# Performance work log

Hardware: AMD Instinct MI355X
Metric: run time of the kernel (lower is better)

## Reference

```python
import jax, jax.numpy as jnp
import numpy as np

N, C, K, H = 131072, 512, 128, 8  # points, channels, patch_size, heads


def setup_inputs() -> dict:
    key = jax.random.key(0)
    ks = jax.random.split(key, 6)
    feat = jax.random.normal(ks[0], (N, C), dtype=jnp.float32)
    Wqkv = jax.random.normal(ks[1], (C, 3 * C), dtype=jnp.float32) * 0.02
    bqkv = jax.random.normal(ks[2], (3 * C,), dtype=jnp.float32) * 0.02
    Wproj = jax.random.normal(ks[3], (C, C), dtype=jnp.float32) * 0.02
    bproj = jax.random.normal(ks[4], (C,), dtype=jnp.float32) * 0.02
    order = jax.random.permutation(ks[5], N).astype(jnp.int64)  # serialized order (all clusters full)
    inverse = jnp.argsort(order).astype(jnp.int64)              # serialized inverse
    return {"feat": feat, "Wqkv": Wqkv, "bqkv": bqkv, "Wproj": Wproj,
            "bproj": bproj, "order": order, "inverse": inverse}


def reference(feat, Wqkv, bqkv, Wproj, bproj, order, inverse):
    hd = C // H
    scale = hd ** -0.5
    qkv = feat @ Wqkv + bqkv                 # [N, 3C]
    qkv = qkv[order]                         # gather by serialized order
    qkv = qkv.reshape(-1, K, 3, H, hd)       # [W, K, 3, H, hd]
    qkv = jnp.moveaxis(qkv, 2, 0)            # [3, W, K, H, hd]
    q = jnp.swapaxes(qkv[0], 1, 2)           # [W, H, K, hd]
    k = jnp.swapaxes(qkv[1], 1, 2)
    v = jnp.swapaxes(qkv[2], 1, 2)
    # upcast_attention / upcast_softmax -> compute scores & softmax in fp32
    attn = jnp.einsum('whkd,whjd->whkj', (q * scale).astype(jnp.float32),
                      k.astype(jnp.float32))             # [W, H, K, K]
    attn = jax.nn.softmax(attn, axis=-1).astype(feat.dtype)
    out = jnp.einsum('whkj,whjd->whkd', attn, v)          # [W, H, K, hd]
    out = jnp.swapaxes(out, 1, 2).reshape(-1, C)          # [N, C]
    out = out[inverse]                                    # scatter back via inverse
    out = out @ Wproj + bproj
    return out
```

## Files before the change

### kernel.cpp

```cpp
#include <hip/hip_runtime.h>
#include <hip/hip_bf16.h>
#include <cstdint>
#include <cstddef>

typedef __bf16 bf16;
typedef __bf16 bf16x8 __attribute__((ext_vector_type(8)));
typedef float f32x4 __attribute__((ext_vector_type(4)));

#define N_PTS 131072
#define CDIM  512
#define C3    1536
#define HD    64
#define NH    8
#define KWIN  128

static __device__ __forceinline__ bf16 cvt(float x) { return (bf16)x; }

static __device__ __forceinline__ void gld16(const bf16* g, bf16* l) {
    __builtin_amdgcn_global_load_lds(
        (const __attribute__((address_space(1))) void*)g,
        (__attribute__((address_space(3))) void*)l, 16, 0, 0);
}

__global__ __launch_bounds__(256) void k_prep(
    const float* __restrict__ Wqkv, const float* __restrict__ Wproj,
    bf16* __restrict__ Wqkv_t, bf16* __restrict__ Wproj_t)
{
    int idx = blockIdx.x * 256 + threadIdx.x;
    if (idx < CDIM * C3) {
        int k = idx / C3, c = idx % C3;
        Wqkv_t[(size_t)c * CDIM + k] = cvt(Wqkv[idx]);
    } else {
        int j = idx - CDIM * C3;
        if (j < CDIM * CDIM) {
            int k = j / CDIM, c = j % CDIM;
            Wproj_t[(size_t)c * CDIM + k] = cvt(Wproj[j]);
        }
    }
}

__global__ __launch_bounds__(256) void k_gather(
    const float* __restrict__ feat, const int* __restrict__ order,
    bf16* __restrict__ feat_g)
{
    int row = blockIdx.x * 2 + (threadIdx.x >> 7);
    int c   = (threadIdx.x & 127) << 2;
    int src = order[row];
    float4 v = *reinterpret_cast<const float4*>(feat + (size_t)src * CDIM + c);
    union { bf16 e[4]; uint2 u; } pk;
    pk.e[0] = cvt(v.x); pk.e[1] = cvt(v.y); pk.e[2] = cvt(v.z); pk.e[3] = cvt(v.w);
    *reinterpret_cast<uint2*>(feat_g + (size_t)row * CDIM + c) = pk.u;
}

template <bool F32OUT, int NT>
__global__ __launch_bounds__(512, 4) void k_gemm(
    const bf16* __restrict__ Ag, const bf16* __restrict__ Bt,
    const float* __restrict__ bias, void* __restrict__ outp)
{
    __shared__ __align__(16) bf16 As[2][128 * 32];
    __shared__ __align__(16) bf16 Bs[2][256 * 32];

    const int t    = threadIdx.x;
    const int lane = t & 63;
    const int wv   = t >> 6;
    const int wr   = wv >> 2;
    const int wc   = wv & 3;
    const int g    = lane >> 4, r16 = lane & 15;

    const int nwg = gridDim.x;
    const int bid = blockIdx.x;
    const int swz = (bid & 7) * (nwg >> 3) + (bid >> 3);
    const int m0  = (swz / NT) * 128;
    const int n0  = (swz % NT) * 256;

    const int L0 = wv * 64 + lane;
    const int rA = L0 >> 2,          sA = ((L0 & 3) - (rA >> 1)) & 3;
    const int rB1 = rA + 128,        sB1v = ((L0 & 3) - (rB1 >> 1)) & 3;
    const bf16* srcA  = Ag + (size_t)(m0 + rA) * CDIM + sA * 8;
    const bf16* srcB0 = Bt + (size_t)(n0 + rA) * CDIM + sA * 8;
    const bf16* srcB1 = Bt + (size_t)(n0 + rB1) * CDIM + sB1v * 8;

    int aoff[4], boff[4];
#pragma unroll
    for (int m = 0; m < 4; ++m) {
        int row = wr * 64 + m * 16 + r16;
        aoff[m] = row * 64 + (((g + (row >> 1)) & 3) << 4);
    }
#pragma unroll
    for (int n = 0; n < 4; ++n) {
        int row = wc * 64 + n * 16 + r16;
        boff[n] = row * 64 + (((g + (row >> 1)) & 3) << 4);
    }

    f32x4 acc[4][4];
    const f32x4 z = {0.f, 0.f, 0.f, 0.f};
#pragma unroll
    for (int m = 0; m < 4; ++m)
#pragma unroll
        for (int n = 0; n < 4; ++n) acc[m][n] = z;

    auto stage = [&](int kt) {
        const int b  = kt & 1;
        const int ko = kt * 32;
        gld16(srcA  + ko, &As[b][(size_t)wv * 64 * 8]);
        gld16(srcB0 + ko, &Bs[b][(size_t)wv * 64 * 8]);
        gld16(srcB1 + ko, &Bs[b][(size_t)(512 + wv * 64) * 8]);
    };

    auto compute = [&](int kt) {
        const int b = kt & 1;
        bf16x8 af[4], bv[4];
#pragma unroll
        for (int m = 0; m < 4; ++m)
            af[m] = *reinterpret_cast<const bf16x8*>(
                reinterpret_cast<const char*>(&As[b][0]) + aoff[m]);
#pragma unroll
        for (int n = 0; n < 4; ++n)
            bv[n] = *reinterpret_cast<const bf16x8*>(
                reinterpret_cast<const char*>(&Bs[b][0]) + boff[n]);
        __builtin_amdgcn_s_setprio(1);
#pragma unroll
        for (int m = 0; m < 4; ++m)
#pragma unroll
            for (int n = 0; n < 4; ++n)
                acc[m][n] = __builtin_amdgcn_mfma_f32_16x16x32_bf16(
                    af[m], bv[n], acc[m][n], 0, 0, 0);
        __builtin_amdgcn_s_setprio(0);
    };

    const int NKT = CDIM / 32;

    stage(0); stage(1);
    asm volatile("s_waitcnt vmcnt(3)" ::: "memory");
    __builtin_amdgcn_s_barrier();

#pragma unroll
    for (int kt = 0; kt < NKT - 2; ++kt) {
        compute(kt);
        asm volatile("s_waitcnt lgkmcnt(0)" ::: "memory");
        __builtin_amdgcn_s_barrier();
        stage(kt + 2);
        asm volatile("s_waitcnt vmcnt(3)" ::: "memory");
        __builtin_amdgcn_s_barrier();
    }
    compute(NKT - 2);
    asm volatile("s_waitcnt vmcnt(0) lgkmcnt(0)" ::: "memory");
    __builtin_amdgcn_s_barrier();
    compute(NKT - 1);

    const int ldo = NT * 256;
#pragma unroll
    for (int n = 0; n < 4; ++n) {
        int col = n0 + wc * 64 + n * 16 + r16;
        float b = bias[col];
#pragma unroll
        for (int m = 0; m < 4; ++m)
#pragma unroll
            for (int j = 0; j < 4; ++j) {
                int row = m0 + wr * 64 + m * 16 + g * 4 + j;
                if (F32OUT)
                    reinterpret_cast<float*>(outp)[(size_t)row * ldo + col] =
                        acc[m][n][j] + b;
                else
                    reinterpret_cast<bf16*>(outp)[(size_t)row * ldo + col] =
                        cvt(acc[m][n][j] + b);
            }
    }
}

__global__ __launch_bounds__(256) void k_attn(
    const bf16* __restrict__ qkv_s, const int* __restrict__ order,
    bf16* __restrict__ attn_g)
{
    __shared__ __align__(16) char smem[36864 + 64 * 136 * 2];
    __shared__ int ord_s[KWIN];
    bf16 (*Q)[72]   = reinterpret_cast<bf16 (*)[72]>(smem);
    bf16 (*Kt)[72]  = reinterpret_cast<bf16 (*)[72]>(smem + 128 * 72 * 2);
    bf16 (*P)[136]  = reinterpret_cast<bf16 (*)[136]>(smem);
    bf16 (*Vt)[136] = reinterpret_cast<bf16 (*)[136]>(smem + 36864);

    const int t    = threadIdx.x;
    const int lane = t & 63;
    const int wv   = t >> 6;
    const int g    = lane >> 4, r16 = lane & 15;
    const int h    = blockIdx.x;
    const int w    = blockIdx.y;

    const bf16* base = qkv_s + (size_t)w * KWIN * C3 + h * HD;

    if (t < KWIN) ord_s[t] = order[w * KWIN + t];

#pragma unroll
    for (int it = 0; it < 4; ++it) {
        int s   = it * 256 + t;
        int tok = s >> 3;
        int c8  = (s & 7) << 3;
        size_t roff = (size_t)tok * C3 + c8;
        *reinterpret_cast<uint4*>(&Q[tok][c8])  =
            *reinterpret_cast<const uint4*>(base + roff);
        *reinterpret_cast<uint4*>(&Kt[tok][c8]) =
            *reinterpret_cast<const uint4*>(base + roff + CDIM);
        uint4 vvec = *reinterpret_cast<const uint4*>(base + roff + 2 * CDIM);
        const bf16* ve = reinterpret_cast<const bf16*>(&vvec);
#pragma unroll
        for (int i = 0; i < 8; ++i) Vt[c8 + i][tok] = ve[i];
    }
    __syncthreads();

    f32x4 sc[2][8];
    const f32x4 z = {0.f, 0.f, 0.f, 0.f};
#pragma unroll
    for (int m = 0; m < 2; ++m)
#pragma unroll
        for (int n = 0; n < 8; ++n) sc[m][n] = z;

#pragma unroll
    for (int ks = 0; ks < 2; ++ks) {
        bf16x8 aq[2];
#pragma unroll
        for (int m = 0; m < 2; ++m)
            aq[m] = *reinterpret_cast<const bf16x8*>(
                &Q[wv * 32 + m * 16 + r16][ks * 32 + g * 8]);
#pragma unroll
        for (int n = 0; n < 8; ++n) {
            bf16x8 bk = *reinterpret_cast<const bf16x8*>(
                &Kt[n * 16 + r16][ks * 32 + g * 8]);
#pragma unroll
            for (int m = 0; m < 2; ++m)
                sc[m][n] = __builtin_amdgcn_mfma_f32_16x16x32_bf16(
                    aq[m], bk, sc[m][n], 0, 0, 0);
        }
    }

    const float scale = 0.125f;
    float inv_sum[2][4];
#pragma unroll
    for (int m = 0; m < 2; ++m) {
#pragma unroll
        for (int j = 0; j < 4; ++j) {
            float mx = -3.0e38f;
#pragma unroll
            for (int n = 0; n < 8; ++n) mx = fmaxf(mx, sc[m][n][j]);
            mx = fmaxf(mx, __shfl_xor(mx, 1));
            mx = fmaxf(mx, __shfl_xor(mx, 2));
            mx = fmaxf(mx, __shfl_xor(mx, 4));
            mx = fmaxf(mx, __shfl_xor(mx, 8));
            mx *= scale;
            float ssum = 0.f;
#pragma unroll
            for (int n = 0; n < 8; ++n) {
                float p = __expf(sc[m][n][j] * scale - mx);
                sc[m][n][j] = p;
                ssum += p;
            }
            ssum += __shfl_xor(ssum, 1);
            ssum += __shfl_xor(ssum, 2);
            ssum += __shfl_xor(ssum, 4);
            ssum += __shfl_xor(ssum, 8);
            inv_sum[m][j] = 1.f / ssum;
        }
    }

    __syncthreads();

#pragma unroll
    for (int m = 0; m < 2; ++m)
#pragma unroll
        for (int n = 0; n < 8; ++n)
#pragma unroll
            for (int j = 0; j < 4; ++j)
                P[wv * 32 + m * 16 + g * 4 + j][n * 16 + r16] =
                    cvt(sc[m][n][j] * inv_sum[m][j]);

    f32x4 o[2][4];
#pragma unroll
    for (int m = 0; m < 2; ++m)
#pragma unroll
        for (int n = 0; n < 4; ++n) o[m][n] = z;

#pragma unroll
    for (int kt = 0; kt < 4; ++kt) {
        bf16x8 ap[2];
#pragma unroll
        for (int m = 0; m < 2; ++m)
            ap[m] = *reinterpret_cast<const bf16x8*>(
                &P[wv * 32 + m * 16 + r16][kt * 32 + g * 8]);
#pragma unroll
        for (int n = 0; n < 4; ++n) {
            bf16x8 bv = *reinterpret_cast<const bf16x8*>(
                &Vt[n * 16 + r16][kt * 32 + g * 8]);
#pragma unroll
            for (int m = 0; m < 2; ++m)
                o[m][n] = __builtin_amdgcn_mfma_f32_16x16x32_bf16(
                    ap[m], bv, o[m][n], 0, 0, 0);
        }
    }

#pragma unroll
    for (int m = 0; m < 2; ++m)
#pragma unroll
        for (int n = 0; n < 4; ++n)
#pragma unroll
            for (int j = 0; j < 4; ++j) {
                int tok  = wv * 32 + m * 16 + g * 4 + j;
                int d    = n * 16 + r16;
                int drow = ord_s[tok];
                attn_g[(size_t)drow * CDIM + h * HD + d] = cvt(o[m][n][j]);
            }
}

extern "C" void kernel_launch(void* const* d_in, const int* in_sizes, int n_in,
                              void* d_out, int out_size, void* d_ws, size_t ws_size,
                              hipStream_t stream)
{
    const float* feat    = (const float*)d_in[0];
    const float* Wqkv    = (const float*)d_in[1];
    const float* bqkv    = (const float*)d_in[2];
    const float* Wproj   = (const float*)d_in[3];
    const float* bproj   = (const float*)d_in[4];
    const int*   order   = (const int*)d_in[5];
    float* out = (float*)d_out;

    const size_t qkv_bytes  = (size_t)N_PTS * C3 * sizeof(bf16);
    const size_t gat_bytes  = (size_t)N_PTS * CDIM * sizeof(bf16);
    const size_t wq_bytes   = (size_t)C3 * CDIM * sizeof(bf16);
    const size_t wp_bytes   = (size_t)CDIM * CDIM * sizeof(bf16);
    if (ws_size < qkv_bytes + gat_bytes + wq_bytes + wp_bytes) return;

    bf16* qkv_s     = (bf16*)d_ws;
    bf16* shared134 = (bf16*)((char*)d_ws + qkv_bytes);
    bf16* Wqkv_t    = (bf16*)((char*)d_ws + qkv_bytes + gat_bytes);
    bf16* Wproj_t   = (bf16*)((char*)d_ws + qkv_bytes + gat_bytes + wq_bytes);

    k_prep<<<dim3((CDIM * C3 + CDIM * CDIM + 255) / 256), 256, 0, stream>>>(
        Wqkv, Wproj, Wqkv_t, Wproj_t);
    k_gather<<<dim3(N_PTS / 2), 256, 0, stream>>>(feat, order, shared134);
    k_gemm<false, C3 / 256><<<dim3((N_PTS / 128) * (C3 / 256)), 512, 0, stream>>>(
        shared134, Wqkv_t, bqkv, qkv_s);
    k_attn<<<dim3(NH, N_PTS / KWIN), 256, 0, stream>>>(qkv_s, order, shared134);
    k_gemm<true, CDIM / 256><<<dim3((N_PTS / 128) * (CDIM / 256)), 512, 0, stream>>>(
        shared134, Wproj_t, bproj, out);
}
```

Before: 640.1 us.

## Fuse row gather and fp32-to-bf16 conversion into QKV GEMM A-tile loading

```diff
diff --git a/kernel.cpp b/kernel.cpp
--- a/kernel.cpp
+++ b/kernel.cpp
@@ -39,26 +39,15 @@
     }
 }
 
-__global__ __launch_bounds__(256) void k_gather(
-    const float* __restrict__ feat, const int* __restrict__ order,
-    bf16* __restrict__ feat_g)
-{
-    int row = blockIdx.x * 2 + (threadIdx.x >> 7);
-    int c   = (threadIdx.x & 127) << 2;
-    int src = order[row];
-    float4 v = *reinterpret_cast<const float4*>(feat + (size_t)src * CDIM + c);
-    union { bf16 e[4]; uint2 u; } pk;
-    pk.e[0] = cvt(v.x); pk.e[1] = cvt(v.y); pk.e[2] = cvt(v.z); pk.e[3] = cvt(v.w);
-    *reinterpret_cast<uint2*>(feat_g + (size_t)row * CDIM + c) = pk.u;
-}
-
-template <bool F32OUT, int NT>
+template <bool GATHER, bool F32OUT, int NT>
 __global__ __launch_bounds__(512, 4) void k_gemm(
-    const bf16* __restrict__ Ag, const bf16* __restrict__ Bt,
-    const float* __restrict__ bias, void* __restrict__ outp)
+    const void* __restrict__ Ag_, const bf16* __restrict__ Bt,
+    const float* __restrict__ bias, const int* __restrict__ order,
+    void* __restrict__ outp)
 {
     __shared__ __align__(16) bf16 As[2][128 * 32];
     __shared__ __align__(16) bf16 Bs[2][256 * 32];
+    __shared__ int ord_s[128];
 
     const int t    = threadIdx.x;
     const int lane = t & 63;
@@ -73,12 +62,25 @@
     const int m0  = (swz / NT) * 128;
     const int n0  = (swz % NT) * 256;
 
-    const int L0 = wv * 64 + lane;
-    const int rA = L0 >> 2,          sA = ((L0 & 3) - (rA >> 1)) & 3;
-    const int rB1 = rA + 128,        sB1v = ((L0 & 3) - (rB1 >> 1)) & 3;
-    const bf16* srcA  = Ag + (size_t)(m0 + rA) * CDIM + sA * 8;
-    const bf16* srcB0 = Bt + (size_t)(n0 + rA) * CDIM + sA * 8;
-    const bf16* srcB1 = Bt + (size_t)(n0 + rB1) * CDIM + sB1v * 8;
+    const float* Af = (const float*)Ag_;
+    const bf16*  Ab = (const bf16*)Ag_;
+    const int NKT = CDIM / 32;
+
+    if (GATHER) {
+        if (t < 128) ord_s[t] = order[m0 + t];
+        __syncthreads();
+    }
+
+    const int rowA = t >> 2;
+    const int ksA  = ((t & 3) - (rowA >> 1)) & 3;
+    const float* gsrcA = GATHER
+        ? Af + (size_t)ord_s[rowA] * CDIM + ksA * 8 : nullptr;
+    const bf16* srcA_l = Ab + (size_t)(m0 + rowA) * CDIM + ksA * 8;
+
+    const int rB0 = t >> 2,        sB0 = ((t & 3) - (rB0 >> 1)) & 3;
+    const int rB1 = rB0 + 128,     sB1 = ((t & 3) - (rB1 >> 1)) & 3;
+    const bf16* srcB0 = Bt + (size_t)(n0 + rB0) * CDIM + sB0 * 8;
+    const bf16* srcB1 = Bt + (size_t)(n0 + rB1) * CDIM + sB1 * 8;
 
     int aoff[4], boff[4];
 #pragma unroll
@@ -99,54 +101,91 @@
 #pragma unroll
         for (int n = 0; n < 4; ++n) acc[m][n] = z;
 
-    auto stage = [&](int kt) {
-        const int b  = kt & 1;
-        const int ko = kt * 32;
-        gld16(srcA  + ko, &As[b][(size_t)wv * 64 * 8]);
-        gld16(srcB0 + ko, &Bs[b][(size_t)wv * 64 * 8]);
-        gld16(srcB1 + ko, &Bs[b][(size_t)(512 + wv * 64) * 8]);
+    auto stageB = [&](int s) {
+        const int b = s & 1;
+        gld16(srcB0 + s * 32, &Bs[b][(size_t)wv * 64 * 8]);
+        gld16(srcB1 + s * 32, &Bs[b][(size_t)(512 + wv * 64) * 8]);
     };
-
-    auto compute = [&](int kt) {
-        const int b = kt & 1;
-        bf16x8 af[4], bv[4];
+    auto stageA_l = [&](int s) {
+        const int b = s & 1;
+        gld16(srcA_l + s * 32, &As[b][(size_t)wv * 64 * 8]);
+    };
+    auto packA = [&](int s, float4 fa, float4 fb) {
+        union { bf16 e[8]; uint4 u; } pk;
+        pk.e[0] = cvt(fa.x); pk.e[1] = cvt(fa.y);
+        pk.e[2] = cvt(fa.z); pk.e[3] = cvt(fa.w);
+        pk.e[4] = cvt(fb.x); pk.e[5] = cvt(fb.y);
+        pk.e[6] = cvt(fb.z); pk.e[7] = cvt(fb.w);
+        *reinterpret_cast<uint4*>(
+            reinterpret_cast<char*>(&As[s & 1][0]) + t * 16) = pk.u;
+    };
+    auto compute = [&](int s) {
+        const int b = s & 1;
+        const char* ab = reinterpret_cast<const char*>(&As[b][0]);
+        const char* bb = reinterpret_cast<const char*>(&Bs[b][0]);
+        bf16x8 af[4], bvv[4];
 #pragma unroll
         for (int m = 0; m < 4; ++m)
-            af[m] = *reinterpret_cast<const bf16x8*>(
-                reinterpret_cast<const char*>(&As[b][0]) + aoff[m]);
+            af[m] = *reinterpret_cast<const bf16x8*>(ab + aoff[m]);
 #pragma unroll
         for (int n = 0; n < 4; ++n)
-            bv[n] = *reinterpret_cast<const bf16x8*>(
-                reinterpret_cast<const char*>(&Bs[b][0]) + boff[n]);
+            bvv[n] = *reinterpret_cast<const bf16x8*>(bb + boff[n]);
         __builtin_amdgcn_s_setprio(1);
 #pragma unroll
         for (int m = 0; m < 4; ++m)
 #pragma unroll
             for (int n = 0; n < 4; ++n)
                 acc[m][n] = __builtin_amdgcn_mfma_f32_16x16x32_bf16(
-                    af[m], bv[n], acc[m][n], 0, 0, 0);
+                    af[m], bvv[n], acc[m][n], 0, 0, 0);
         __builtin_amdgcn_s_setprio(0);
     };
 
-    const int NKT = CDIM / 32;
-
-    stage(0); stage(1);
-    asm volatile("s_waitcnt vmcnt(3)" ::: "memory");
-    __builtin_amdgcn_s_barrier();
-
-#pragma unroll
-    for (int kt = 0; kt < NKT - 2; ++kt) {
-        compute(kt);
+    if (GATHER) {
+        float4 fa0 = *reinterpret_cast<const float4*>(gsrcA);
+        float4 fb0 = *reinterpret_cast<const float4*>(gsrcA + 4);
+        float4 fa1 = *reinterpret_cast<const float4*>(gsrcA + 32);
+        float4 fb1 = *reinterpret_cast<const float4*>(gsrcA + 36);
+        stageB(0); stageB(1);
+        packA(0, fa0, fb0);
+        packA(1, fa1, fb1);
+        asm volatile("s_waitcnt vmcnt(2) lgkmcnt(0)" ::: "memory");
+        __builtin_amdgcn_s_barrier();
+    } else {
+        stageA_l(0); stageB(0);
+        stageA_l(1); stageB(1);
+        asm volatile("s_waitcnt vmcnt(3)" ::: "memory");
+        __builtin_amdgcn_s_barrier();
+    }
+
+#pragma unroll
+    for (int s = 0; s < NKT; ++s) {
+        float4 fa, fb;
+        if (GATHER && s + 2 < NKT) {
+            fa = *reinterpret_cast<const float4*>(gsrcA + (s + 2) * 32);
+            fb = *reinterpret_cast<const float4*>(gsrcA + (s + 2) * 32 + 4);
+        }
+        compute(s);
+        if (s == NKT - 1) break;
         asm volatile("s_waitcnt lgkmcnt(0)" ::: "memory");
         __builtin_amdgcn_s_barrier();
-        stage(kt + 2);
-        asm volatile("s_waitcnt vmcnt(3)" ::: "memory");
+        if (GATHER) {
+            if (s + 2 < NKT) {
+                packA(s + 2, fa, fb);
+                stageB(s + 2);
+                asm volatile("s_waitcnt lgkmcnt(0)" ::: "memory");
+            } else {
+                asm volatile("s_waitcnt vmcnt(0)" ::: "memory");
+            }
+        } else {
+            if (s + 2 < NKT) {
+                stageA_l(s + 2); stageB(s + 2);
+                asm volatile("s_waitcnt vmcnt(3)" ::: "memory");
+            } else {
+                asm volatile("s_waitcnt vmcnt(0)" ::: "memory");
+            }
+        }
         __builtin_amdgcn_s_barrier();
     }
-    compute(NKT - 2);
-    asm volatile("s_waitcnt vmcnt(0) lgkmcnt(0)" ::: "memory");
-    __builtin_amdgcn_s_barrier();
-    compute(NKT - 1);
 
     const int ldo = NT * 256;
 #pragma unroll
@@ -287,12 +326,12 @@
                 &P[wv * 32 + m * 16 + r16][kt * 32 + g * 8]);
 #pragma unroll
         for (int n = 0; n < 4; ++n) {
-            bf16x8 bv = *reinterpret_cast<const bf16x8*>(
+            bf16x8 bvv = *reinterpret_cast<const bf16x8*>(
                 &Vt[n * 16 + r16][kt * 32 + g * 8]);
 #pragma unroll
             for (int m = 0; m < 2; ++m)
                 o[m][n] = __builtin_amdgcn_mfma_f32_16x16x32_bf16(
-                    ap[m], bv, o[m][n], 0, 0, 0);
+                    ap[m], bvv, o[m][n], 0, 0, 0);
         }
     }
 
@@ -327,17 +366,18 @@
     const size_t wp_bytes   = (size_t)CDIM * CDIM * sizeof(bf16);
     if (ws_size < qkv_bytes + gat_bytes + wq_bytes + wp_bytes) return;
 
-    bf16* qkv_s     = (bf16*)d_ws;
-    bf16* shared134 = (bf16*)((char*)d_ws + qkv_bytes);
-    bf16* Wqkv_t    = (bf16*)((char*)d_ws + qkv_bytes + gat_bytes);
-    bf16* Wproj_t   = (bf16*)((char*)d_ws + qkv_bytes + gat_bytes + wq_bytes);
+    bf16* qkv_s   = (bf16*)d_ws;
+    bf16* attn_g  = (bf16*)((char*)d_ws + qkv_bytes);
+    bf16* Wqkv_t  = (bf16*)((char*)d_ws + qkv_bytes + gat_bytes);
+    bf16* Wproj_t = (bf16*)((char*)d_ws + qkv_bytes + gat_bytes + wq_bytes);
 
     k_prep<<<dim3((CDIM * C3 + CDIM * CDIM + 255) / 256), 256, 0, stream>>>(
         Wqkv, Wproj, Wqkv_t, Wproj_t);
-    k_gather<<<dim3(N_PTS / 2), 256, 0, stream>>>(feat, order, shared134);
-    k_gemm<false, C3 / 256><<<dim3((N_PTS / 128) * (C3 / 256)), 512, 0, stream>>>(
-        shared134, Wqkv_t, bqkv, qkv_s);
-    k_attn<<<dim3(NH, N_PTS / KWIN), 256, 0, stream>>>(qkv_s, order, shared134);
-    k_gemm<true, CDIM / 256><<<dim3((N_PTS / 128) * (CDIM / 256)), 512, 0, stream>>>(
-        shared134, Wproj_t, bproj, out);
-}
+    k_gemm<true, false, C3 / 256>
+        <<<dim3((N_PTS / 128) * (C3 / 256)), 512, 0, stream>>>(
+        feat, Wqkv_t, bqkv, order, qkv_s);
+    k_attn<<<dim3(NH, N_PTS / KWIN), 256, 0, stream>>>(qkv_s, order, attn_g);
+    k_gemm<false, true, CDIM / 256>
+        <<<dim3((N_PTS / 128) * (CDIM / 256)), 512, 0, stream>>>(
+        attn_g, Wproj_t, bproj, order, out);
+}
```

Result: faster. 598.0 us (-6.6%).

## Restructure GEMM to 128x128 tiles with triple-buffered LDS and register prefetch

Applied to the files above, without the earlier changes.

```diff
diff --git a/kernel.cpp b/kernel.cpp
--- a/kernel.cpp
+++ b/kernel.cpp
@@ -53,32 +53,34 @@
 }
 
 template <bool F32OUT, int NT>
-__global__ __launch_bounds__(512, 4) void k_gemm(
+__global__ __launch_bounds__(256, 3) void k_gemm(
     const bf16* __restrict__ Ag, const bf16* __restrict__ Bt,
     const float* __restrict__ bias, void* __restrict__ outp)
 {
-    __shared__ __align__(16) bf16 As[2][128 * 32];
-    __shared__ __align__(16) bf16 Bs[2][256 * 32];
+    __shared__ __align__(16) bf16 As[3][128 * 32];
+    __shared__ __align__(16) bf16 Bs[3][128 * 32];
 
     const int t    = threadIdx.x;
     const int lane = t & 63;
     const int wv   = t >> 6;
-    const int wr   = wv >> 2;
-    const int wc   = wv & 3;
+    const int wr   = wv >> 1;
+    const int wc   = wv & 1;
     const int g    = lane >> 4, r16 = lane & 15;
 
     const int nwg = gridDim.x;
     const int bid = blockIdx.x;
     const int swz = (bid & 7) * (nwg >> 3) + (bid >> 3);
     const int m0  = (swz / NT) * 128;
-    const int n0  = (swz % NT) * 256;
-
-    const int L0 = wv * 64 + lane;
-    const int rA = L0 >> 2,          sA = ((L0 & 3) - (rA >> 1)) & 3;
-    const int rB1 = rA + 128,        sB1v = ((L0 & 3) - (rB1 >> 1)) & 3;
-    const bf16* srcA  = Ag + (size_t)(m0 + rA) * CDIM + sA * 8;
-    const bf16* srcB0 = Bt + (size_t)(n0 + rA) * CDIM + sA * 8;
-    const bf16* srcB1 = Bt + (size_t)(n0 + rB1) * CDIM + sB1v * 8;
+    const int n0  = (swz % NT) * 128;
+
+    const int NKT = CDIM / 32;
+
+    const int r0 = t >> 2,       s0 = ((t & 3) - (r0 >> 1)) & 3;
+    const int r1 = r0 + 64,      s1 = ((t & 3) - (r1 >> 1)) & 3;
+    const bf16* srcA0 = Ag + (size_t)(m0 + r0) * CDIM + s0 * 8;
+    const bf16* srcA1 = Ag + (size_t)(m0 + r1) * CDIM + s1 * 8;
+    const bf16* srcB0 = Bt + (size_t)(n0 + r0) * CDIM + s0 * 8;
+    const bf16* srcB1 = Bt + (size_t)(n0 + r1) * CDIM + s1 * 8;
 
     int aoff[4], boff[4];
 #pragma unroll
@@ -99,56 +101,58 @@
 #pragma unroll
         for (int n = 0; n < 4; ++n) acc[m][n] = z;
 
-    auto stage = [&](int kt) {
-        const int b  = kt & 1;
-        const int ko = kt * 32;
-        gld16(srcA  + ko, &As[b][(size_t)wv * 64 * 8]);
-        gld16(srcB0 + ko, &Bs[b][(size_t)wv * 64 * 8]);
-        gld16(srcB1 + ko, &Bs[b][(size_t)(512 + wv * 64) * 8]);
+    auto stage = [&](int s) {
+        const int b  = s % 3;
+        const int ko = s * 32;
+        gld16(srcA0 + ko, &As[b][(size_t)(wv * 64) * 8]);
+        gld16(srcA1 + ko, &As[b][(size_t)(wv * 64 + 256) * 8]);
+        gld16(srcB0 + ko, &Bs[b][(size_t)(wv * 64) * 8]);
+        gld16(srcB1 + ko, &Bs[b][(size_t)(wv * 64 + 256) * 8]);
     };
 
-    auto compute = [&](int kt) {
-        const int b = kt & 1;
-        bf16x8 af[4], bv[4];
+    bf16x8 afr[2][4], bfr[2][4];
+
+    auto ldfrags = [&](int set, int b) {
+        const char* ab = reinterpret_cast<const char*>(&As[b][0]);
+        const char* bb = reinterpret_cast<const char*>(&Bs[b][0]);
 #pragma unroll
         for (int m = 0; m < 4; ++m)
-            af[m] = *reinterpret_cast<const bf16x8*>(
-                reinterpret_cast<const char*>(&As[b][0]) + aoff[m]);
+            afr[set][m] = *reinterpret_cast<const bf16x8*>(ab + aoff[m]);
 #pragma unroll
         for (int n = 0; n < 4; ++n)
-            bv[n] = *reinterpret_cast<const bf16x8*>(
-                reinterpret_cast<const char*>(&Bs[b][0]) + boff[n]);
+            bfr[set][n] = *reinterpret_cast<const bf16x8*>(bb + boff[n]);
+    };
+
+    stage(0); stage(1);
+    asm volatile("s_waitcnt vmcnt(4)" ::: "memory");
+    __builtin_amdgcn_s_barrier();
+    ldfrags(0, 0);
+    asm volatile("s_waitcnt lgkmcnt(0)" ::: "memory");
+
+#pragma unroll
+    for (int s = 0; s < NKT; ++s) {
+        if (s + 2 < NKT) stage(s + 2);
+        if (s < NKT - 1) {
+            if (s + 2 < NKT)
+                asm volatile("s_waitcnt vmcnt(4)" ::: "memory");
+            else
+                asm volatile("s_waitcnt vmcnt(0)" ::: "memory");
+            __builtin_amdgcn_s_barrier();
+            ldfrags((s + 1) & 1, (s + 1) % 3);
+        }
         __builtin_amdgcn_s_setprio(1);
 #pragma unroll
         for (int m = 0; m < 4; ++m)
 #pragma unroll
             for (int n = 0; n < 4; ++n)
                 acc[m][n] = __builtin_amdgcn_mfma_f32_16x16x32_bf16(
-                    af[m], bv[n], acc[m][n], 0, 0, 0);
+                    afr[s & 1][m], bfr[s & 1][n], acc[m][n], 0, 0, 0);
         __builtin_amdgcn_s_setprio(0);
-    };
-
-    const int NKT = CDIM / 32;
-
-    stage(0); stage(1);
-    asm volatile("s_waitcnt vmcnt(3)" ::: "memory");
-    __builtin_amdgcn_s_barrier();
-
-#pragma unroll
-    for (int kt = 0; kt < NKT - 2; ++kt) {
-        compute(kt);
-        asm volatile("s_waitcnt lgkmcnt(0)" ::: "memory");
-        __builtin_amdgcn_s_barrier();
-        stage(kt + 2);
-        asm volatile("s_waitcnt vmcnt(3)" ::: "memory");
-        __builtin_amdgcn_s_barrier();
-    }
-    compute(NKT - 2);
-    asm volatile("s_waitcnt vmcnt(0) lgkmcnt(0)" ::: "memory");
-    __builtin_amdgcn_s_barrier();
-    compute(NKT - 1);
-
-    const int ldo = NT * 256;
+        if (s < NKT - 1)
+            asm volatile("s_waitcnt lgkmcnt(0)" ::: "memory");
+    }
+
+    const int ldo = NT * 128;
 #pragma unroll
     for (int n = 0; n < 4; ++n) {
         int col = n0 + wc * 64 + n * 16 + r16;
@@ -287,12 +291,12 @@
                 &P[wv * 32 + m * 16 + r16][kt * 32 + g * 8]);
 #pragma unroll
         for (int n = 0; n < 4; ++n) {
-            bf16x8 bv = *reinterpret_cast<const bf16x8*>(
+            bf16x8 bvv = *reinterpret_cast<const bf16x8*>(
                 &Vt[n * 16 + r16][kt * 32 + g * 8]);
 #pragma unroll
             for (int m = 0; m < 2; ++m)
                 o[m][n] = __builtin_amdgcn_mfma_f32_16x16x32_bf16(
-                    ap[m], bv, o[m][n], 0, 0, 0);
+                    ap[m], bvv, o[m][n], 0, 0, 0);
         }
     }
 
@@ -321,10 +325,10 @@
     const int*   order   = (const int*)d_in[5];
     float* out = (float*)d_out;
 
-    const size_t qkv_bytes  = (size_t)N_PTS * C3 * sizeof(bf16);
-    const size_t gat_bytes  = (size_t)N_PTS * CDIM * sizeof(bf16);
-    const size_t wq_bytes   = (size_t)C3 * CDIM * sizeof(bf16);
-    const size_t wp_bytes   = (size_t)CDIM * CDIM * sizeof(bf16);
+    const size_t qkv_bytes = (size_t)N_PTS * C3 * sizeof(bf16);
+    const size_t gat_bytes = (size_t)N_PTS * CDIM * sizeof(bf16);
+    const size_t wq_bytes  = (size_t)C3 * CDIM * sizeof(bf16);
+    const size_t wp_bytes  = (size_t)CDIM * CDIM * sizeof(bf16);
     if (ws_size < qkv_bytes + gat_bytes + wq_bytes + wp_bytes) return;
 
     bf16* qkv_s     = (bf16*)d_ws;
@@ -335,9 +339,9 @@
     k_prep<<<dim3((CDIM * C3 + CDIM * CDIM + 255) / 256), 256, 0, stream>>>(
         Wqkv, Wproj, Wqkv_t, Wproj_t);
     k_gather<<<dim3(N_PTS / 2), 256, 0, stream>>>(feat, order, shared134);
-    k_gemm<false, C3 / 256><<<dim3((N_PTS / 128) * (C3 / 256)), 512, 0, stream>>>(
+    k_gemm<false, C3 / 128><<<dim3((N_PTS / 128) * (C3 / 128)), 256, 0, stream>>>(
         shared134, Wqkv_t, bqkv, qkv_s);
     k_attn<<<dim3(NH, N_PTS / KWIN), 256, 0, stream>>>(qkv_s, order, shared134);
-    k_gemm<true, CDIM / 256><<<dim3((N_PTS / 128) * (CDIM / 256)), 512, 0, stream>>>(
+    k_gemm<true, CDIM / 128><<<dim3((N_PTS / 128) * (CDIM / 128)), 256, 0, stream>>>(
         shared134, Wproj_t, bproj, out);
 }
```

After: 671.3 us. 1.05x slower.

## Pre-swizzle QKV GEMM operands into MFMA fragment layout and load directly to registers

Applied to the files above, without the earlier changes.

```diff
diff --git a/kernel.cpp b/kernel.cpp
--- a/kernel.cpp
+++ b/kernel.cpp
@@ -13,6 +13,7 @@
 #define HD    64
 #define NH    8
 #define KWIN  128
+#define NKS   16
 
 static __device__ __forceinline__ bf16 cvt(float x) { return (bf16)x; }
 
@@ -22,34 +23,120 @@
         (__attribute__((address_space(3))) void*)l, 16, 0, 0);
 }
 
+
 __global__ __launch_bounds__(256) void k_prep(
     const float* __restrict__ Wqkv, const float* __restrict__ Wproj,
-    bf16* __restrict__ Wqkv_t, bf16* __restrict__ Wproj_t)
-{
-    int idx = blockIdx.x * 256 + threadIdx.x;
-    if (idx < CDIM * C3) {
-        int k = idx / C3, c = idx % C3;
-        Wqkv_t[(size_t)c * CDIM + k] = cvt(Wqkv[idx]);
+    bf16* __restrict__ Wq_frag, bf16* __restrict__ Wp_t)
+{
+    const int b = blockIdx.x, t = threadIdx.x;
+    if (b < 384) {
+        int slot  = b * 256 + t;
+        int chunk = slot >> 6;
+        int l     = slot & 63;
+        int cf = chunk >> 4, ks = chunk & 15;
+        int col = cf * 16 + (l & 15);
+        int kb  = ks * 32 + (l >> 4) * 8;
+        union { bf16 e[8]; uint4 u; } pk;
+#pragma unroll
+        for (int ei = 0; ei < 8; ++ei)
+            pk.e[ei] = cvt(Wqkv[(size_t)(kb + ei) * C3 + col]);
+        *reinterpret_cast<uint4*>(Wq_frag + (size_t)chunk * 512 + l * 8) = pk.u;
     } else {
-        int j = idx - CDIM * C3;
-        if (j < CDIM * CDIM) {
-            int k = j / CDIM, c = j % CDIM;
-            Wproj_t[(size_t)c * CDIM + k] = cvt(Wproj[j]);
-        }
+        int j = (b - 384) * 256 + t;
+        int k = j >> 9, c = j & 511;
+        Wp_t[(size_t)c * CDIM + k] = cvt(Wproj[(size_t)k * CDIM + c]);
     }
 }
 
 __global__ __launch_bounds__(256) void k_gather(
     const float* __restrict__ feat, const int* __restrict__ order,
-    bf16* __restrict__ feat_g)
-{
-    int row = blockIdx.x * 2 + (threadIdx.x >> 7);
-    int c   = (threadIdx.x & 127) << 2;
-    int src = order[row];
-    float4 v = *reinterpret_cast<const float4*>(feat + (size_t)src * CDIM + c);
-    union { bf16 e[4]; uint2 u; } pk;
-    pk.e[0] = cvt(v.x); pk.e[1] = cvt(v.y); pk.e[2] = cvt(v.z); pk.e[3] = cvt(v.w);
-    *reinterpret_cast<uint2*>(feat_g + (size_t)row * CDIM + c) = pk.u;
+    bf16* __restrict__ Afrag)
+{
+    const int rf = blockIdx.x;
+    const int t = threadIdx.x, wv = t >> 6, l = t & 63;
+    const int srow = order[rf * 16 + (l & 15)];
+    const float* src = feat + (size_t)srow * CDIM + (l >> 4) * 8;
+#pragma unroll
+    for (int q = 0; q < 4; ++q) {
+        int ks = wv * 4 + q;
+        float4 v0 = *reinterpret_cast<const float4*>(src + ks * 32);
+        float4 v1 = *reinterpret_cast<const float4*>(src + ks * 32 + 4);
+        union { bf16 e[8]; uint4 u; } pk;
+        pk.e[0] = cvt(v0.x); pk.e[1] = cvt(v0.y);
+        pk.e[2] = cvt(v0.z); pk.e[3] = cvt(v0.w);
+        pk.e[4] = cvt(v1.x); pk.e[5] = cvt(v1.y);
+        pk.e[6] = cvt(v1.z); pk.e[7] = cvt(v1.w);
+        *reinterpret_cast<uint4*>(
+            Afrag + ((size_t)rf * 16 + ks) * 512 + l * 8) = pk.u;
+    }
+}
+
+template <int NT>
+__global__ __launch_bounds__(512, 2) void k_mm_frag(
+    const bf16* __restrict__ Afrag, const bf16* __restrict__ Bfrag,
+    const float* __restrict__ bias, bf16* __restrict__ outp)
+{
+    const int t    = threadIdx.x;
+    const int lane = t & 63;
+    const int wv   = t >> 6;
+    const int wr   = wv >> 2;
+    const int wc   = wv & 3;
+    const int g    = lane >> 4, r16 = lane & 15;
+
+    const int nwg = gridDim.x;
+    const int bid = blockIdx.x;
+    const int swz = (bid & 7) * (nwg >> 3) + (bid >> 3);
+    const int m0  = (swz / NT) * 256;
+    const int n0  = (swz % NT) * 256;
+
+    const bf16* pA = Afrag + (size_t)(m0 / 16 + wr * 8) * 8192 + lane * 8;
+    const bf16* pB = Bfrag + (size_t)(n0 / 16 + wc * 4) * 8192 + lane * 8;
+
+    f32x4 acc[8][4];
+    const f32x4 z = {0.f, 0.f, 0.f, 0.f};
+#pragma unroll
+    for (int i = 0; i < 8; ++i)
+#pragma unroll
+        for (int n = 0; n < 4; ++n) acc[i][n] = z;
+
+    bf16x8 aR[2][8], bR[2][4];
+
+    auto LD = [&](int set, int ks) {
+#pragma unroll
+        for (int i = 0; i < 8; ++i)
+            aR[set][i] = *reinterpret_cast<const bf16x8*>(pA + i * 8192 + ks * 512);
+#pragma unroll
+        for (int n = 0; n < 4; ++n)
+            bR[set][n] = *reinterpret_cast<const bf16x8*>(pB + n * 8192 + ks * 512);
+    };
+
+    LD(0, 0);
+#pragma unroll
+    for (int ks = 0; ks < NKS; ++ks) {
+        if (ks + 1 < NKS) LD((ks + 1) & 1, ks + 1);
+        __builtin_amdgcn_s_setprio(1);
+#pragma unroll
+        for (int i = 0; i < 8; ++i)
+#pragma unroll
+            for (int n = 0; n < 4; ++n)
+                acc[i][n] = __builtin_amdgcn_mfma_f32_16x16x32_bf16(
+                    aR[ks & 1][i], bR[ks & 1][n], acc[i][n], 0, 0, 0);
+        __builtin_amdgcn_s_setprio(0);
+    }
+
+    const int ldo = NT * 256;
+#pragma unroll
+    for (int n = 0; n < 4; ++n) {
+        int col = n0 + wc * 64 + n * 16 + r16;
+        float b = bias[col];
+#pragma unroll
+        for (int i = 0; i < 8; ++i)
+#pragma unroll
+            for (int j = 0; j < 4; ++j) {
+                int row = m0 + wr * 128 + i * 16 + g * 4 + j;
+                outp[(size_t)row * ldo + col] = cvt(acc[i][n][j] + b);
+            }
+    }
 }
 
 template <bool F32OUT, int NT>
@@ -109,14 +196,14 @@
 
     auto compute = [&](int kt) {
         const int b = kt & 1;
-        bf16x8 af[4], bv[4];
+        bf16x8 af[4], bvv[4];
 #pragma unroll
         for (int m = 0; m < 4; ++m)
             af[m] = *reinterpret_cast<const bf16x8*>(
                 reinterpret_cast<const char*>(&As[b][0]) + aoff[m]);
 #pragma unroll
         for (int n = 0; n < 4; ++n)
-            bv[n] = *reinterpret_cast<const bf16x8*>(
+            bvv[n] = *reinterpret_cast<const bf16x8*>(
                 reinterpret_cast<const char*>(&Bs[b][0]) + boff[n]);
         __builtin_amdgcn_s_setprio(1);
 #pragma unroll
@@ -124,7 +211,7 @@
 #pragma unroll
             for (int n = 0; n < 4; ++n)
                 acc[m][n] = __builtin_amdgcn_mfma_f32_16x16x32_bf16(
-                    af[m], bv[n], acc[m][n], 0, 0, 0);
+                    af[m], bvv[n], acc[m][n], 0, 0, 0);
         __builtin_amdgcn_s_setprio(0);
     };
 
@@ -287,12 +374,12 @@
                 &P[wv * 32 + m * 16 + r16][kt * 32 + g * 8]);
 #pragma unroll
         for (int n = 0; n < 4; ++n) {
-            bf16x8 bv = *reinterpret_cast<const bf16x8*>(
+            bf16x8 bvv = *reinterpret_cast<const bf16x8*>(
                 &Vt[n * 16 + r16][kt * 32 + g * 8]);
 #pragma unroll
             for (int m = 0; m < 2; ++m)
                 o[m][n] = __builtin_amdgcn_mfma_f32_16x16x32_bf16(
-                    ap[m], bv, o[m][n], 0, 0, 0);
+                    ap[m], bvv, o[m][n], 0, 0, 0);
         }
     }
 
@@ -321,23 +408,22 @@
     const int*   order   = (const int*)d_in[5];
     float* out = (float*)d_out;
 
-    const size_t qkv_bytes  = (size_t)N_PTS * C3 * sizeof(bf16);
-    const size_t gat_bytes  = (size_t)N_PTS * CDIM * sizeof(bf16);
-    const size_t wq_bytes   = (size_t)C3 * CDIM * sizeof(bf16);
-    const size_t wp_bytes   = (size_t)CDIM * CDIM * sizeof(bf16);
+    const size_t qkv_bytes = (size_t)N_PTS * C3 * sizeof(bf16);
+    const size_t gat_bytes = (size_t)N_PTS * CDIM * sizeof(bf16);
+    const size_t wq_bytes  = (size_t)C3 * CDIM * sizeof(bf16);
+    const size_t wp_bytes  = (size_t)CDIM * CDIM * sizeof(bf16);
     if (ws_size < qkv_bytes + gat_bytes + wq_bytes + wp_bytes) return;
 
     bf16* qkv_s     = (bf16*)d_ws;
     bf16* shared134 = (bf16*)((char*)d_ws + qkv_bytes);
-    bf16* Wqkv_t    = (bf16*)((char*)d_ws + qkv_bytes + gat_bytes);
-    bf16* Wproj_t   = (bf16*)((char*)d_ws + qkv_bytes + gat_bytes + wq_bytes);
-
-    k_prep<<<dim3((CDIM * C3 + CDIM * CDIM + 255) / 256), 256, 0, stream>>>(
-        Wqkv, Wproj, Wqkv_t, Wproj_t);
-    k_gather<<<dim3(N_PTS / 2), 256, 0, stream>>>(feat, order, shared134);
-    k_gemm<false, C3 / 256><<<dim3((N_PTS / 128) * (C3 / 256)), 512, 0, stream>>>(
-        shared134, Wqkv_t, bqkv, qkv_s);
+    bf16* Wq_frag   = (bf16*)((char*)d_ws + qkv_bytes + gat_bytes);
+    bf16* Wp_t      = (bf16*)((char*)d_ws + qkv_bytes + gat_bytes + wq_bytes);
+
+    k_prep<<<dim3(384 + 1024), 256, 0, stream>>>(Wqkv, Wproj, Wq_frag, Wp_t);
+    k_gather<<<dim3(N_PTS / 16), 256, 0, stream>>>(feat, order, shared134);
+    k_mm_frag<C3 / 256><<<dim3((N_PTS / 256) * (C3 / 256)), 512, 0, stream>>>(
+        shared134, Wq_frag, bqkv, qkv_s);
     k_attn<<<dim3(NH, N_PTS / KWIN), 256, 0, stream>>>(qkv_s, order, shared134);
     k_gemm<true, CDIM / 256><<<dim3((N_PTS / 128) * (CDIM / 256)), 512, 0, stream>>>(
-        shared134, Wproj_t, bproj, out);
-}
+        shared134, Wp_t, bproj, out);
+}
```

Result: slower. 882.5 us (+37.9%).
